# Kernel optimization log

Hardware: AMD Instinct MI355X
Metric: run time of the kernel (lower is better)

## Reference

```python
import jax, jax.numpy as jnp
import numpy as np

K = 20
NEG_SLOPE = 0.2
BN_EPS = 1e-5


def knn_idx(x, k):
    # x: (B, C, N) -> neighbor indices (B, N, k) by largest negative sq-distance
    xt = jnp.swapaxes(x, 1, 2)                      # (B, N, C)
    inner = 2.0 * jnp.einsum('bic,bjc->bij', xt, xt)
    sq = jnp.sum(xt * xt, axis=-1)                  # (B, N)
    dist = inner - sq[:, :, None] - sq[:, None, :]  # -||xi-xj||^2
    _, idx = jax.lax.top_k(dist, k)
    return idx


def edge_feature(x, src, idx):
    # x: (B, C, N) centers; src: (B, C, M) gather source; idx: (B, N, k)
    xt = jnp.swapaxes(x, 1, 2)                      # (B, N, C)
    st = jnp.swapaxes(src, 1, 2)                    # (B, M, C)
    b = jnp.arange(xt.shape[0])[:, None, None]
    neigh = st[b, idx]                              # (B, N, k, C)
    center = xt[:, :, None, :]                      # (B, N, 1, C)
    feat = jnp.concatenate(
        [neigh - center, jnp.broadcast_to(center, neigh.shape)], axis=-1)
    return jnp.transpose(feat, (0, 3, 1, 2))        # (B, 2C, N, k)


def conv_bn_lrelu(x, w, gamma, beta):
    # 1x1 conv (no bias) + training-mode BatchNorm2d + LeakyReLU(0.2)
    y = jnp.einsum('oc,bcnk->bonk', w, x)
    mean = jnp.mean(y, axis=(0, 2, 3), keepdims=True)
    var = jnp.var(y, axis=(0, 2, 3), keepdims=True)
    y = (y - mean) * jax.lax.rsqrt(var + BN_EPS)
    y = y * gamma[None, :, None, None] + beta[None, :, None, None]
    return jnp.where(y >= 0, y, NEG_SLOPE * y)


def knn_ia_idx(x, y, k):
    # cosine-similarity KNN from x (B,Cx,N) into y (B,Cy,M), normalize over channels
    xn = x / jnp.maximum(jnp.linalg.norm(x, axis=1, keepdims=True), 1e-12)
    yn = y / jnp.maximum(jnp.linalg.norm(y, axis=1, keepdims=True), 1e-12)
    simi = jnp.einsum('bci,bcj->bij', xn, yn)       # (B, N, M)
    _, idx = jax.lax.top_k(simi, k)
    return idx


def setup_inputs() -> dict:
    key = jax.random.key(0)
    ks = jax.random.split(key, 8)
    B, N, M, EMB = 8, 1024, 1024, 512
    x = jax.random.normal(ks[0], (B, 3, N), dtype=jnp.float32)
    y = jax.random.normal(ks[1], (B, 128, M), dtype=jnp.float32)
    def w(k_, o, c):
        return jax.random.normal(k_, (o, c), dtype=jnp.float32) * (1.0 / np.sqrt(c))
    inp = {
        'x': x, 'y': y,
        'w1': w(ks[2], 64, 6),
        'w2': w(ks[3], 64, 128),
        'w3': w(ks[4], 128, 128),
        'w4': w(ks[5], 256, 256),
        'w5': w(ks[6], EMB, 512),
        'g1': jnp.ones(64), 'b1': jnp.zeros(64),
        'g2': jnp.ones(64), 'b2': jnp.zeros(64),
        'g3': jnp.ones(128), 'b3': jnp.zeros(128),
        'g4': jnp.ones(256), 'b4': jnp.zeros(256),
        'g5': jnp.ones(EMB), 'b5': jnp.zeros(EMB),
    }
    return inp


def reference(x, y, w1, w2, w3, w4, w5, g1, b1, g2, b2, g3, b3, g4, b4, g5, b5):
    # block 1
    h = conv_bn_lrelu(edge_feature(x, x, knn_idx(x, K)), w1, g1, b1)
    x1 = jnp.max(h, axis=-1)                        # (B, 64, N)
    # block 2
    h = conv_bn_lrelu(edge_feature(x1, x1, knn_idx(x1, K)), w2, g2, b2)
    x2 = jnp.max(h, axis=-1)                        # (B, 64, N)
    # block 3
    h = conv_bn_lrelu(edge_feature(x2, x2, knn_idx(x2, K)), w3, g3, b3)
    x3 = jnp.max(h, axis=-1)                        # (B, 128, N)
    # block 4: cross-attention KNN into y (cosine similarity)
    h = conv_bn_lrelu(edge_feature(x3, y, knn_ia_idx(x3, y, K)), w4, g4, b4)
    x4 = jnp.max(h, axis=-1)                        # (B, 256, N)
    # final 1x1 conv + BN + LeakyReLU on concatenated features (512 ch)
    cat = jnp.concatenate([x1, x2, x3, x4], axis=1)  # (B, 512, N)
    out = conv_bn_lrelu(cat[..., None], w5, g5, b5)[..., 0]
    return out                                       # (B, n_emb_dims, N)
```

## Files before the change

kernel.cpp:

```cpp
#include <hip/hip_runtime.h>
#include <hip/hip_bf16.h>

#define KNN 20
#define NEG_SLOPE 0.2f

constexpr int BB = 8;
constexpr int NN = 1024;
constexpr int MM = 1024;

typedef short bf16x8 __attribute__((ext_vector_type(8)));
typedef float f32x4 __attribute__((ext_vector_type(4)));

__device__ __forceinline__ unsigned pack_key(double d, int j) {
  float f = (float)d;
  unsigned u = __float_as_uint(f);
  u = (u & 0x80000000u) ? ~u : (u | 0x80000000u);
  return (u & ~1023u) | (unsigned)(1023 - j);
}

__device__ __forceinline__ void topk_exact_f64(double (&v)[16], int lane, int* op) {
  for (int r = 0; r < KNN; ++r) {
    double bv = -INFINITY;
    int bj = MM;
#pragma unroll
    for (int m = 0; m < 16; ++m) {
      if (v[m] > bv) { bv = v[m]; bj = m * 64 + lane; }
    }
#pragma unroll
    for (int off = 32; off > 0; off >>= 1) {
      double ov = __shfl_xor(bv, off, 64);
      int oj = __shfl_xor(bj, off, 64);
      if (ov > bv || (ov == bv && oj < bj)) { bv = ov; bj = oj; }
    }
    if (bj < MM && lane == (bj & 63)) v[bj >> 6] = -INFINITY;
    if (lane == 0) op[r] = bj;
  }
}

__device__ __forceinline__ bool topk20_fast(unsigned (&s)[16], int lane, int* op) {
#pragma unroll
  for (int p = 1; p < 16; p <<= 1) {
#pragma unroll
    for (int k = p; k >= 1; k >>= 1) {
#pragma unroll
      for (int j = k % p; j + k < 16; j += 2 * k) {
#pragma unroll
        for (int i = 0; i < k; ++i) {
          int a = j + i, b = j + i + k;
          if (b < 16 && (a / (2 * p)) == (b / (2 * p))) {
            unsigned hi = s[a] > s[b] ? s[a] : s[b];
            unsigned lo = s[a] > s[b] ? s[b] : s[a];
            s[a] = hi;
            s[b] = lo;
          }
        }
      }
    }
  }
  unsigned prev = 0;
#pragma unroll
  for (int r = 0; r < KNN; ++r) {
    unsigned win = s[0];
#pragma unroll
    for (int off = 32; off > 0; off >>= 1) {
      unsigned o = __shfl_xor(win, off, 64);
      win = o > win ? o : win;
    }
    if (lane == 0) op[r] = 1023 - (int)(win & 1023u);
    if (s[0] == win) {
#pragma unroll
      for (int i = 0; i < 15; ++i) s[i] = s[i + 1];
      s[15] = 0u;
    }
    prev = win;
  }
  unsigned win21 = s[0];
#pragma unroll
  for (int off = 32; off > 0; off >>= 1) {
    unsigned o = __shfl_xor(win21, off, 64);
    win21 = o > win21 ? o : win21;
  }
  return (prev >> 10) == (win21 >> 10);
}

__global__ __launch_bounds__(256) void k_transpose_d(
    const float* __restrict__ in, double* __restrict__ out, int C, int Np) {
  int total = BB * C * Np;
  for (int t = blockIdx.x * 256 + threadIdx.x; t < total; t += gridDim.x * 256) {
    int c = t % C;
    int n = (t / C) % Np;
    int b = t / (C * Np);
    out[t] = (double)in[((size_t)b * C + c) * Np + n];
  }
}

__global__ __launch_bounds__(256) void k_cvt_bf16(
    const float* __restrict__ in, __hip_bfloat16* __restrict__ out, int n) {
  int i = blockIdx.x * 256 + threadIdx.x;
  if (i < n) out[i] = __float2bfloat16(in[i]);
}

template <int RECIP>
__global__ __launch_bounds__(256) void k_rowsq(
    const double* __restrict__ A, int ld, int C, double* __restrict__ sq) {
  int p = blockIdx.x * 256 + threadIdx.x;
  if (p >= BB * NN) return;
  const double* row = A + (size_t)p * ld;
  double s = 0.0;
  for (int c = 0; c < C; ++c) { double v = row[c]; s += v * v; }
  if (RECIP) {
    sq[p] = 1.0 / fmax(sqrt(s), 1e-12);
  } else {
    sq[p] = s;
  }
}

__global__ __launch_bounds__(256) void k_knn3(
    const double* __restrict__ xs3, const double* __restrict__ sq, int* __restrict__ idx) {
  __shared__ double P[NN * 3];
  int b = blockIdx.x;
  const double* Xb = xs3 + (size_t)b * NN * 3;
  int tid = threadIdx.x;
  for (int t = tid; t < NN * 3; t += 256) P[t] = Xb[t];
  __syncthreads();
  int wave = tid >> 6, lane = tid & 63;
  int i = blockIdx.y * 4 + wave;
  double xi = P[i * 3], yi = P[i * 3 + 1], zi = P[i * 3 + 2];
  double sqi = sq[b * NN + i];
  double v[16];
  unsigned s[16];
#pragma unroll
  for (int m = 0; m < 16; ++m) {
    int j = m * 64 + lane;
    double d = fma(xi, P[j * 3], 0.0);
    d = fma(yi, P[j * 3 + 1], d);
    d = fma(zi, P[j * 3 + 2], d);
    v[m] = 2.0 * d - sqi - sq[b * NN + j];
    s[m] = pack_key(v[m], j);
  }
  int* op = idx + ((size_t)b * NN + i) * KNN;
  if (topk20_fast(s, lane, op)) topk_exact_f64(v, lane, op);
}

template <int MODE>
__global__ __launch_bounds__(256) void k_gram2(
    const double* __restrict__ A, int lda, const double* __restrict__ Bm, int ldb,
    const double* __restrict__ sqA, const double* __restrict__ sqB,
    double* __restrict__ D, unsigned* __restrict__ kk, int C, int b0) {
  __shared__ double As[16][137];
  __shared__ double Bs[16][73];
  int bg = b0 + blockIdx.x;
  int bl = blockIdx.x;
  int j0 = blockIdx.y * 64;
  int i0 = blockIdx.z * 128;
  const double* Ab = A + (size_t)bg * NN * lda;
  const double* Bb = Bm + (size_t)bg * MM * ldb;
  int tx = threadIdx.x, ty = threadIdx.y;
  int tid = ty * 16 + tx;
  double acc[8][4] = {};
  for (int c0 = 0; c0 < C; c0 += 16) {
    for (int r = 0; r < 2; ++r) {
      int li = tid + r * 256;
      int row = li >> 2;
      int f = (li & 3) * 4;
      const double* ap = &Ab[(size_t)(i0 + row) * lda + c0 + f];
      double2 a0 = *(const double2*)ap;
      double2 a1 = *(const double2*)(ap + 2);
      As[f + 0][row] = a0.x;
      As[f + 1][row] = a0.y;
      As[f + 2][row] = a1.x;
      As[f + 3][row] = a1.y;
    }
    {
      int row = tid >> 2;
      int f = (tid & 3) * 4;
      const double* bp = &Bb[(size_t)(j0 + row) * ldb + c0 + f];
      double2 b0v = *(const double2*)bp;
      double2 b1v = *(const double2*)(bp + 2);
      Bs[f + 0][row] = b0v.x;
      Bs[f + 1][row] = b0v.y;
      Bs[f + 2][row] = b1v.x;
      Bs[f + 3][row] = b1v.y;
    }
    __syncthreads();
#pragma unroll
    for (int k = 0; k < 16; ++k) {
      double a_[8], b_[4];
#pragma unroll
      for (int ii = 0; ii < 8; ++ii) a_[ii] = As[k][ty * 8 + ii];
#pragma unroll
      for (int jj = 0; jj < 4; ++jj) b_[jj] = Bs[k][jj * 16 + tx];
#pragma unroll
      for (int ii = 0; ii < 8; ++ii)
#pragma unroll
        for (int jj = 0; jj < 4; ++jj)
          acc[ii][jj] = fma(a_[ii], b_[jj], acc[ii][jj]);
    }
    __syncthreads();
  }
  for (int ii = 0; ii < 8; ++ii) {
    int i = i0 + ty * 8 + ii;
    for (int jj = 0; jj < 4; ++jj) {
      int j = j0 + jj * 16 + tx;
      double r = acc[ii][jj];
      if (MODE == 1) r = 2.0 * r - sqA[bg * NN + i] - sqB[bg * NN + j];
      if (MODE == 2) r = r * sqA[bg * NN + i] * sqB[bg * NN + j];
      size_t o = ((size_t)bl * NN + i) * MM + j;
      D[o] = r;
      kk[o] = pack_key(r, j);
    }
  }
}

__global__ __launch_bounds__(256) void k_gram_sym(
    const double* __restrict__ A, int lda, const double* __restrict__ sqA,
    double* __restrict__ D, unsigned* __restrict__ kk, int C, int b0) {
  __shared__ double As[16][69];
  __shared__ double Bs[16][69];
  __shared__ double T[64][65];
  int p = blockIdx.y;
  int r = (int)((sqrtf(8.f * p + 1.f) - 1.f) * 0.5f);
  while ((r + 1) * (r + 2) / 2 <= p) ++r;
  while (r * (r + 1) / 2 > p) --r;
  int cc = p - r * (r + 1) / 2;
  int i0 = r * 64, j0 = cc * 64;
  int bg = b0 + blockIdx.x;
  int bl = blockIdx.x;
  const double* Ab = A + (size_t)bg * NN * lda;
  int tx = threadIdx.x, ty = threadIdx.y;
  int tid = ty * 16 + tx;
  double acc[4][4] = {};
  for (int c0 = 0; c0 < C; c0 += 16) {
    for (int rr = 0; rr < 4; ++rr) {
      int li = tid + rr * 256;
      int row = li >> 4, k = li & 15;
      int c = c0 + k;
      As[k][row] = (c < C) ? Ab[(size_t)(i0 + row) * lda + c] : 0.0;
      Bs[k][row] = (c < C) ? Ab[(size_t)(j0 + row) * lda + c] : 0.0;
    }
    __syncthreads();
#pragma unroll
    for (int k = 0; k < 16; ++k) {
      double a_[4], b_[4];
#pragma unroll
      for (int ii = 0; ii < 4; ++ii) a_[ii] = As[k][ty * 4 + ii];
#pragma unroll
      for (int jj = 0; jj < 4; ++jj) b_[jj] = Bs[k][jj * 16 + tx];
#pragma unroll
      for (int ii = 0; ii < 4; ++ii)
#pragma unroll
        for (int jj = 0; jj < 4; ++jj)
          acc[ii][jj] = fma(a_[ii], b_[jj], acc[ii][jj]);
    }
    __syncthreads();
  }
  for (int ii = 0; ii < 4; ++ii) {
    int i = i0 + ty * 4 + ii;
    for (int jj = 0; jj < 4; ++jj) {
      int j = j0 + jj * 16 + tx;
      double v = 2.0 * acc[ii][jj] - sqA[bg * NN + i] - sqA[bg * NN + j];
      size_t o = ((size_t)bl * NN + i) * MM + j;
      D[o] = v;
      kk[o] = pack_key(v, j);
      T[jj * 16 + tx][ty * 4 + ii] = v;
    }
  }
  if (i0 != j0) {
    __syncthreads();
    for (int rr = 0; rr < 16; ++rr) {
      int li = tid + rr * 256;
      int jrow = li >> 6, il = li & 63;
      double v = T[jrow][il];
      size_t o = ((size_t)bl * NN + j0 + jrow) * MM + i0 + il;
      D[o] = v;
      kk[o] = pack_key(v, i0 + il);
    }
  }
}

__global__ __launch_bounds__(256) void k_topk(const unsigned* __restrict__ kk,
                                              const double* __restrict__ D,
                                              int* __restrict__ idx, int b0) {
  int wave = threadIdx.x >> 6;
  int lane = threadIdx.x & 63;
  int bl = blockIdx.x;
  int row = blockIdx.y * 4 + wave;
  const unsigned* rp = kk + ((size_t)bl * NN + row) * MM;
  unsigned s[16];
#pragma unroll
  for (int m = 0; m < 16; ++m) s[m] = rp[m * 64 + lane];
  int* op = idx + ((size_t)(b0 + bl) * NN + row) * KNN;
  if (topk20_fast(s, lane, op)) {
    const double* dp = D + ((size_t)bl * NN + row) * MM;
    double v[16];
#pragma unroll
    for (int m = 0; m < 16; ++m) v[m] = dp[m * 64 + lane];
    topk_exact_f64(v, lane, op);
  }
}

__global__ __launch_bounds__(256) void k_featmm2(
    const double* __restrict__ src0, int ld0, int Np0,
    const double* __restrict__ src1, int ld1,
    const float* __restrict__ w, int CW,
    double* __restrict__ out0, double* __restrict__ out1, int C, int O) {
  __shared__ double As[16][68];
  __shared__ double Ws[16][68];
  int nbo = O >> 6;
  int b = blockIdx.x;
  int mode = blockIdx.y >= nbo;
  int o0 = (blockIdx.y - (mode ? nbo : 0)) * 64;
  int j0 = blockIdx.z * 64;
  const double* src = mode ? src1 : src0;
  int lds_ = mode ? ld1 : ld0;
  int Np = mode ? NN : Np0;
  double* out = mode ? out1 : out0;
  int tx = threadIdx.x, ty = threadIdx.y;
  int tid = ty * 16 + tx;
  const double* Sb = src + (size_t)b * Np * lds_;
  double acc[4][4] = {};
  for (int c0 = 0; c0 < C; c0 += 16) {
    for (int r = 0; r < 4; ++r) {
      int li = tid + r * 256;
      int row = li >> 4, k = li & 15;
      int c = c0 + k;
      As[k][row] = (c < C) ? Sb[(size_t)(j0 + row) * lds_ + c] : 0.0;
      double wv = 0.0;
      if (c < C) {
        const float* wr = w + (size_t)(o0 + row) * CW;
        wv = (mode == 0) ? (double)wr[c] : ((double)wr[C + c] - (double)wr[c]);
      }
      Ws[k][row] = wv;
    }
    __syncthreads();
#pragma unroll
    for (int k = 0; k < 16; ++k) {
      double a_[4], b_[4];
#pragma unroll
      for (int ii = 0; ii < 4; ++ii) a_[ii] = As[k][ty * 4 + ii];
#pragma unroll
      for (int jj = 0; jj < 4; ++jj) b_[jj] = Ws[k][tx * 4 + jj];
#pragma unroll
      for (int ii = 0; ii < 4; ++ii)
#pragma unroll
        for (int jj = 0; jj < 4; ++jj)
          acc[ii][jj] = fma(a_[ii], b_[jj], acc[ii][jj]);
    }
    __syncthreads();
  }
  for (int ii = 0; ii < 4; ++ii) {
    int j = j0 + ty * 4 + ii;
    double* op = &out[((size_t)b * Np + j) * O + o0 + tx * 4];
    double2 v0, v1;
    v0.x = acc[ii][0];
    v0.y = acc[ii][1];
    v1.x = acc[ii][2];
    v1.y = acc[ii][3];
    *(double2*)op = v0;
    *(double2*)(op + 2) = v1;
  }
}

__global__ __launch_bounds__(256) void k_gemm5_mfma(
    const __hip_bfloat16* __restrict__ cath, const __hip_bfloat16* __restrict__ w5h,
    float* __restrict__ out) {
  int b = blockIdx.x;
  int j0 = blockIdx.y * 16;
  int o0 = blockIdx.z * 64 + (threadIdx.x >> 6) * 16;
  int lane = threadIdx.x & 63;
  int m = lane & 15;
  int quad = lane >> 4;
  const __hip_bfloat16* arow = cath + ((size_t)b * NN + j0 + m) * 512 + quad * 8;
  const __hip_bfloat16* brow = w5h + (size_t)(o0 + m) * 512 + quad * 8;
  f32x4 acc = {0.f, 0.f, 0.f, 0.f};
#pragma unroll
  for (int c0 = 0; c0 < 512; c0 += 32) {
    bf16x8 a = *(const bf16x8*)(arow + c0);
    bf16x8 bb = *(const bf16x8*)(brow + c0);
    acc = __builtin_amdgcn_mfma_f32_16x16x32_bf16(a, bb, acc, 0, 0, 0);
  }
  float* obase = &out[((size_t)b * NN + j0 + quad * 4) * 512 + o0 + m];
#pragma unroll
  for (int r = 0; r < 4; ++r) obase[(size_t)r * 512] = acc[r];
}

__global__ __launch_bounds__(256) void k_gather(
    const double* __restrict__ u, const double* __restrict__ t, const int* __restrict__ idx,
    double* __restrict__ stats, double* __restrict__ mx, int O, int srcNp) {
  __shared__ int lidx[16 * KNN];
  __shared__ double rs[256];
  __shared__ double rq[256];
  int b = blockIdx.x;
  int n0 = blockIdx.y * 16;
  int o0 = blockIdx.z * 64;
  int tid = threadIdx.x;
  int lane = tid & 63, nsl = tid >> 6;
  for (int w = tid; w < 16 * KNN; w += 256)
    lidx[w] = idx[((size_t)b * NN + n0) * KNN + w];
  __syncthreads();
  int oo = o0 + lane;
  double s1 = 0.0, s2 = 0.0;
  for (int ns = nsl; ns < 16; ns += 4) {
    size_t row = (size_t)b * NN + n0 + ns;
    double tv = t[row * O + oo];
    double mxv = -INFINITY;
    double a1 = 0.0, a2 = 0.0;
#pragma unroll
    for (int k = 0; k < KNN; ++k) {
      int j = lidx[ns * KNN + k];
      double yv = u[((size_t)b * srcNp + j) * O + oo] + tv;
      mxv = fmax(mxv, yv);
      a1 += yv;
      a2 = fma(yv, yv, a2);
    }
    mx[row * O + oo] = mxv;
    s1 += a1;
    s2 += a2;
  }
  rs[tid] = s1;
  rq[tid] = s2;
  __syncthreads();
  if (tid < 64) {
    s1 = rs[tid] + rs[tid + 64] + rs[tid + 128] + rs[tid + 192];
    s2 = rq[tid] + rq[tid + 64] + rq[tid + 128] + rq[tid + 192];
    atomicAdd(&stats[o0 + tid], s1);
    atomicAdd(&stats[O + o0 + tid], s2);
  }
}

__global__ void k_bnfin(const double* __restrict__ stats, const float* __restrict__ gamma,
                        const float* __restrict__ beta, double* __restrict__ sc,
                        int O, double cnt) {
  int o = threadIdx.x;
  if (o >= O) return;
  double mean = stats[o] / cnt;
  double var = stats[O + o] / cnt - mean * mean;
  if (var < 0.0) var = 0.0;
  double rstd = 1.0 / sqrt(var + 1e-5);
  double s = (double)gamma[o] * rstd;
  double c = (double)beta[o] - mean * s;
  sc[o] = s;
  sc[O + o] = c;
}

__global__ __launch_bounds__(256) void k_bnapply(
    const double* __restrict__ mx, const double* __restrict__ u, const double* __restrict__ t,
    const int* __restrict__ idx, const double* __restrict__ sc, double* __restrict__ catd,
    __hip_bfloat16* __restrict__ cath, int coff, int O, int srcNp) {
  int i = blockIdx.x * 256 + threadIdx.x;
  int total = BB * NN * O;
  if (i >= total) return;
  int oo = i % O;
  int n = (i / O) % NN;
  int b = i / (O * NN);
  double s = sc[oo], c = sc[O + oo];
  double v;
  if (s >= 0.0) {
    v = mx[i];
  } else {
    double tv = t[i];
    double mn = INFINITY;
    for (int k = 0; k < KNN; ++k) {
      int j = idx[((size_t)b * NN + n) * KNN + k];
      mn = fmin(mn, u[((size_t)b * srcNp + j) * O + oo] + tv);
    }
    v = mn;
  }
  double a = s * v + c;
  a = (a >= 0.0) ? a : 0.2 * a;
  size_t ci = ((size_t)b * NN + n) * 512 + coff + oo;
  cath[ci] = __float2bfloat16((float)a);
  if (coff < 256) catd[((size_t)b * NN + n) * 256 + coff + oo] = a;
}

__global__ __launch_bounds__(256) void k_stats512(
    const float* __restrict__ y5, double* __restrict__ stats) {
  int b = blockIdx.y;
  int n0 = blockIdx.x * 32;
  int tid = threadIdx.x;
  for (int part = 0; part < 2; ++part) {
    int oo = tid + part * 256;
    float a1 = 0.f, a2 = 0.f;
    for (int ns = 0; ns < 32; ++ns) {
      float v = y5[((size_t)b * NN + n0 + ns) * 512 + oo];
      a1 += v;
      a2 = fmaf(v, v, a2);
    }
    atomicAdd(&stats[oo], (double)a1);
    atomicAdd(&stats[512 + oo], (double)a2);
  }
}

__global__ __launch_bounds__(256) void k_final5b(
    const float* __restrict__ y5, const double* __restrict__ sc, float* __restrict__ out) {
  __shared__ float tile[64][65];
  int b = blockIdx.z;
  int n0 = blockIdx.x * 64;
  int o0 = blockIdx.y * 64;
  int tid = threadIdx.x;
  for (int r = 0; r < 16; ++r) {
    int li = tid + r * 256;
    int nl = li >> 6, ol = li & 63;
    float v = y5[((size_t)b * NN + n0 + nl) * 512 + o0 + ol];
    float a = (float)(sc[o0 + ol] * (double)v + sc[512 + o0 + ol]);
    a = (a >= 0.f) ? a : NEG_SLOPE * a;
    tile[nl][ol] = a;
  }
  __syncthreads();
  for (int r = 0; r < 16; ++r) {
    int li = tid + r * 256;
    int ol = li >> 6, nl = li & 63;
    out[((size_t)b * 512 + o0 + ol) * NN + n0 + nl] = tile[nl][ol];
  }
}

extern "C" void kernel_launch(void* const* d_in, const int* in_sizes, int n_in,
                              void* d_out, int out_size, void* d_ws, size_t ws_size,
                              hipStream_t stream) {
  const float* x = (const float*)d_in[0];
  const float* y = (const float*)d_in[1];
  const float* w1 = (const float*)d_in[2];
  const float* w2 = (const float*)d_in[3];
  const float* w3 = (const float*)d_in[4];
  const float* w4 = (const float*)d_in[5];
  const float* w5 = (const float*)d_in[6];
  const float* g1 = (const float*)d_in[7];
  const float* b1 = (const float*)d_in[8];
  const float* g2 = (const float*)d_in[9];
  const float* b2 = (const float*)d_in[10];
  const float* g3 = (const float*)d_in[11];
  const float* b3 = (const float*)d_in[12];
  const float* g4 = (const float*)d_in[13];
  const float* b4 = (const float*)d_in[14];
  const float* g5 = (const float*)d_in[15];
  const float* b5 = (const float*)d_in[16];

  char* base = (char*)d_ws;
  size_t off = 0;
  auto alloc = [&](size_t bytes) -> char* {
    char* p = base + off;
    off += (bytes + 255) & ~(size_t)255;
    return p;
  };
  double* st = (double*)alloc(1024 * 8);
  double* sc = (double*)alloc(1024 * 8);
  double* sq = (double*)alloc((size_t)BB * NN * 8);
  double* rnx = (double*)alloc((size_t)BB * NN * 8);
  double* rny = (double*)alloc((size_t)BB * MM * 8);
  int* idxb = (int*)alloc((size_t)BB * NN * KNN * 4);
  double* xs3d = (double*)alloc((size_t)BB * NN * 3 * 8);
  double* ysd = (double*)alloc((size_t)BB * MM * 128 * 8);
  double* catd = (double*)alloc((size_t)BB * NN * 256 * 8);
  __hip_bfloat16* cath = (__hip_bfloat16*)alloc((size_t)BB * NN * 512 * 2);
  __hip_bfloat16* w5h = (__hip_bfloat16*)alloc((size_t)512 * 512 * 2);
  double* uu = (double*)alloc((size_t)BB * MM * 256 * 8);
  double* tt = (double*)alloc((size_t)BB * NN * 256 * 8);
  size_t ddBatchBytes = (size_t)NN * MM * 8;
  size_t kkBatchBytes = (size_t)NN * MM * 4;
  size_t avail = (ws_size > off) ? (ws_size - off) : 0;
  int CB = (int)(avail / (ddBatchBytes + kkBatchBytes));
  if (CB < 1) CB = 1;
  if (CB > BB) CB = BB;
  char* U = alloc((size_t)CB * ddBatchBytes);
  unsigned* KK = (unsigned*)alloc((size_t)CB * kkBatchBytes);
  double* DD = (double*)U;
  float* y5 = (float*)uu;
  double* mx = (double*)d_out;
  float* outp = (float*)d_out;

  const dim3 blk2(16, 16);
  const double cntE = (double)BB * NN * KNN;

  auto knn = [&](const double* A, int lda, const double* Bm, int ldb,
                 const double* sa, const double* sb, int C, int mode, int sym) {
    for (int b0 = 0; b0 < BB; b0 += CB) {
      int cb = (BB - b0 < CB) ? (BB - b0) : CB;
      if (sym) {
        k_gram_sym<<<dim3(cb, 136), blk2, 0, stream>>>(A, lda, sa, DD, KK, C, b0);
      } else {
        dim3 g(cb, MM / 64, NN / 128);
        if (mode == 1)
          k_gram2<1><<<g, blk2, 0, stream>>>(A, lda, Bm, ldb, sa, sb, DD, KK, C, b0);
        else
          k_gram2<2><<<g, blk2, 0, stream>>>(A, lda, Bm, ldb, sa, sb, DD, KK, C, b0);
      }
      k_topk<<<dim3(cb, 256), 256, 0, stream>>>(KK, DD, idxb, b0);
    }
  };

  auto edge_layer = [&](const double* ctr, int ldc, const double* src, int ldsrc,
                        int srcNp, const float* w, int CW, const float* g,
                        const float* bb, int C, int O, int coff) {
    k_featmm2<<<dim3(8, 2 * (O / 64), 16), blk2, 0, stream>>>(src, ldsrc, srcNp, ctr,
                                                              ldc, w, CW, uu, tt, C, O);
    hipMemsetAsync(st, 0, 1024 * 8, stream);
    k_gather<<<dim3(BB, NN / 16, O / 64), 256, 0, stream>>>(uu, tt, idxb, st, mx, O,
                                                            srcNp);
    k_bnfin<<<1, O, 0, stream>>>(st, g, bb, sc, O, cntE);
    k_bnapply<<<(BB * NN * O + 255) / 256, 256, 0, stream>>>(mx, uu, tt, idxb, sc, catd,
                                                             cath, coff, O, srcNp);
  };

  k_transpose_d<<<96, 256, 0, stream>>>(x, xs3d, 3, NN);
  k_transpose_d<<<2048, 256, 0, stream>>>(y, ysd, 128, MM);
  k_cvt_bf16<<<1024, 256, 0, stream>>>(w5, w5h, 512 * 512);

  k_rowsq<0><<<32, 256, 0, stream>>>(xs3d, 3, 3, sq);
  k_knn3<<<dim3(BB, 256), 256, 0, stream>>>(xs3d, sq, idxb);
  edge_layer(xs3d, 3, xs3d, 3, NN, w1, 6, g1, b1, 3, 64, 0);

  k_rowsq<0><<<32, 256, 0, stream>>>(catd, 256, 64, sq);
  knn(catd, 256, catd, 256, sq, sq, 64, 1, 1);
  edge_layer(catd, 256, catd, 256, NN, w2, 128, g2, b2, 64, 64, 64);

  k_rowsq<0><<<32, 256, 0, stream>>>(catd + 64, 256, 64, sq);
  knn(catd + 64, 256, catd + 64, 256, sq, sq, 64, 1, 1);
  edge_layer(catd + 64, 256, catd + 64, 256, NN, w3, 128, g3, b3, 64, 128, 128);

  k_rowsq<1><<<32, 256, 0, stream>>>(catd + 128, 256, 128, rnx);
  k_rowsq<1><<<32, 256, 0, stream>>>(ysd, 128, 128, rny);
  knn(catd + 128, 256, ysd, 128, rnx, rny, 128, 2, 0);
  edge_layer(catd + 128, 256, ysd, 128, MM, w4, 256, g4, b4, 128, 256, 256);

  hipMemsetAsync(st, 0, 1024 * 8, stream);
  k_gemm5_mfma<<<dim3(BB, 64, 8), 256, 0, stream>>>(cath, w5h, y5);
  k_stats512<<<dim3(32, 8), 256, 0, stream>>>(y5, st);
  k_bnfin<<<1, 512, 0, stream>>>(st, g5, b5, sc, 512, (double)(BB * NN));
  k_final5b<<<dim3(16, 8, 8), 256, 0, stream>>>(y5, sc, outp);
}
```

Measured before the change: 719.5 us.

## Use FP64 MFMA for KNN gram and recompute exact distances in top-k fallback

Replaces the FP64 FMA gram kernels (including the symmetric variant) with one kernel that uses the 16x16x4 FP64 MFMA instruction. The output lane layout is found at runtime by a probe kernel, and the old FMA path is kept as a fallback. The full double-precision distance matrix is no longer written. The exact top-k fallback instead recomputes the needed row of distances from the input features, which cuts global memory traffic and frees workspace for larger batch chunks. The cost is giving up the symmetric-tile saving, adding two tiny probe launches, and doing redundant row recomputation whenever the fast path fails.

```diff
diff --git a/kernel.cpp b/kernel.cpp
--- a/kernel.cpp
+++ b/kernel.cpp
@@ -10,6 +10,7 @@
 
 typedef short bf16x8 __attribute__((ext_vector_type(8)));
 typedef float f32x4 __attribute__((ext_vector_type(4)));
+typedef double f64x4 __attribute__((ext_vector_type(4)));
 
 __device__ __forceinline__ unsigned pack_key(double d, int j) {
   float f = (float)d;
@@ -81,6 +82,45 @@
     win21 = o > win21 ? o : win21;
   }
   return (prev >> 10) == (win21 >> 10);
+}
+
+__global__ void k_probe_mfma(double* __restrict__ p) {
+  int lane = threadIdx.x & 63;
+  f64x4 z = {0.0, 0.0, 0.0, 0.0};
+  double ai = (double)(lane & 15);
+  double p3 = 1.0, p5 = 1.0;
+  int kq = lane >> 4;
+  for (int t = 0; t < kq; ++t) { p3 *= 3.0; p5 *= 5.0; }
+  f64x4 d1 = __builtin_amdgcn_mfma_f64_16x16x4f64(ai, 1.0, z, 0, 0, 0);
+  f64x4 d2 = __builtin_amdgcn_mfma_f64_16x16x4f64(1.0, ai, z, 0, 0, 0);
+  f64x4 d3 = __builtin_amdgcn_mfma_f64_16x16x4f64(p3, p5, z, 0, 0, 0);
+#pragma unroll
+  for (int r = 0; r < 4; ++r) {
+    p[lane * 4 + r] = d1[r];
+    p[256 + lane * 4 + r] = d2[r];
+    p[512 + lane * 4 + r] = d3[r];
+  }
+}
+
+__global__ void k_probe_decode(const double* __restrict__ p, int* __restrict__ rowt,
+                               int* __restrict__ colt, int* __restrict__ flag) {
+  if (threadIdx.x != 0 || blockIdx.x != 0) return;
+  unsigned char seen[256];
+  for (int e = 0; e < 256; ++e) seen[e] = 0;
+  bool ok = true;
+  for (int e = 0; e < 256 && ok; ++e) {
+    double va = p[e], vb = p[256 + e], vp = p[512 + e];
+    int i = (int)(va * 0.25);
+    int j = (int)(vb * 0.25);
+    ok = (i >= 0) && (i < 16) && (j >= 0) && (j < 16) && (va == 4.0 * (double)i) &&
+         (vb == 4.0 * (double)j) && (vp == 3616.0) && (seen[i * 16 + j] == 0);
+    if (ok) {
+      seen[i * 16 + j] = 1;
+      rowt[e] = i;
+      colt[e] = j;
+    }
+  }
+  *flag = ok ? 1 : 0;
 }
 
 __global__ __launch_bounds__(256) void k_transpose_d(
@@ -143,158 +183,135 @@
 }
 
 template <int MODE>
-__global__ __launch_bounds__(256) void k_gram2(
+__global__ __launch_bounds__(256) void k_gram_u(
     const double* __restrict__ A, int lda, const double* __restrict__ Bm, int ldb,
     const double* __restrict__ sqA, const double* __restrict__ sqB,
-    double* __restrict__ D, unsigned* __restrict__ kk, int C, int b0) {
-  __shared__ double As[16][137];
-  __shared__ double Bs[16][73];
+    unsigned* __restrict__ kk, int C, int b0, const int* __restrict__ rowt,
+    const int* __restrict__ colt, const int* __restrict__ flag) {
+  __shared__ double As[16][66];
+  __shared__ double Bs[16][66];
   int bg = b0 + blockIdx.x;
   int bl = blockIdx.x;
   int j0 = blockIdx.y * 64;
-  int i0 = blockIdx.z * 128;
+  int i0 = blockIdx.z * 64;
   const double* Ab = A + (size_t)bg * NN * lda;
   const double* Bb = Bm + (size_t)bg * MM * ldb;
-  int tx = threadIdx.x, ty = threadIdx.y;
-  int tid = ty * 16 + tx;
-  double acc[8][4] = {};
-  for (int c0 = 0; c0 < C; c0 += 16) {
-    for (int r = 0; r < 2; ++r) {
-      int li = tid + r * 256;
-      int row = li >> 2;
-      int f = (li & 3) * 4;
-      const double* ap = &Ab[(size_t)(i0 + row) * lda + c0 + f];
-      double2 a0 = *(const double2*)ap;
-      double2 a1 = *(const double2*)(ap + 2);
-      As[f + 0][row] = a0.x;
-      As[f + 1][row] = a0.y;
-      As[f + 2][row] = a1.x;
-      As[f + 3][row] = a1.y;
-    }
-    {
-      int row = tid >> 2;
-      int f = (tid & 3) * 4;
-      const double* bp = &Bb[(size_t)(j0 + row) * ldb + c0 + f];
-      double2 b0v = *(const double2*)bp;
-      double2 b1v = *(const double2*)(bp + 2);
-      Bs[f + 0][row] = b0v.x;
-      Bs[f + 1][row] = b0v.y;
-      Bs[f + 2][row] = b1v.x;
-      Bs[f + 3][row] = b1v.y;
-    }
-    __syncthreads();
-#pragma unroll
-    for (int k = 0; k < 16; ++k) {
-      double a_[8], b_[4];
-#pragma unroll
-      for (int ii = 0; ii < 8; ++ii) a_[ii] = As[k][ty * 8 + ii];
-#pragma unroll
-      for (int jj = 0; jj < 4; ++jj) b_[jj] = Bs[k][jj * 16 + tx];
-#pragma unroll
-      for (int ii = 0; ii < 8; ++ii)
-#pragma unroll
-        for (int jj = 0; jj < 4; ++jj)
-          acc[ii][jj] = fma(a_[ii], b_[jj], acc[ii][jj]);
-    }
-    __syncthreads();
-  }
-  for (int ii = 0; ii < 8; ++ii) {
-    int i = i0 + ty * 8 + ii;
-    for (int jj = 0; jj < 4; ++jj) {
-      int j = j0 + jj * 16 + tx;
-      double r = acc[ii][jj];
-      if (MODE == 1) r = 2.0 * r - sqA[bg * NN + i] - sqB[bg * NN + j];
-      if (MODE == 2) r = r * sqA[bg * NN + i] * sqB[bg * NN + j];
-      size_t o = ((size_t)bl * NN + i) * MM + j;
-      D[o] = r;
-      kk[o] = pack_key(r, j);
-    }
-  }
-}
-
-__global__ __launch_bounds__(256) void k_gram_sym(
-    const double* __restrict__ A, int lda, const double* __restrict__ sqA,
-    double* __restrict__ D, unsigned* __restrict__ kk, int C, int b0) {
-  __shared__ double As[16][69];
-  __shared__ double Bs[16][69];
-  __shared__ double T[64][65];
-  int p = blockIdx.y;
-  int r = (int)((sqrtf(8.f * p + 1.f) - 1.f) * 0.5f);
-  while ((r + 1) * (r + 2) / 2 <= p) ++r;
-  while (r * (r + 1) / 2 > p) --r;
-  int cc = p - r * (r + 1) / 2;
-  int i0 = r * 64, j0 = cc * 64;
-  int bg = b0 + blockIdx.x;
-  int bl = blockIdx.x;
-  const double* Ab = A + (size_t)bg * NN * lda;
-  int tx = threadIdx.x, ty = threadIdx.y;
-  int tid = ty * 16 + tx;
-  double acc[4][4] = {};
-  for (int c0 = 0; c0 < C; c0 += 16) {
-    for (int rr = 0; rr < 4; ++rr) {
-      int li = tid + rr * 256;
-      int row = li >> 4, k = li & 15;
-      int c = c0 + k;
-      As[k][row] = (c < C) ? Ab[(size_t)(i0 + row) * lda + c] : 0.0;
-      Bs[k][row] = (c < C) ? Ab[(size_t)(j0 + row) * lda + c] : 0.0;
-    }
-    __syncthreads();
-#pragma unroll
-    for (int k = 0; k < 16; ++k) {
-      double a_[4], b_[4];
-#pragma unroll
-      for (int ii = 0; ii < 4; ++ii) a_[ii] = As[k][ty * 4 + ii];
-#pragma unroll
-      for (int jj = 0; jj < 4; ++jj) b_[jj] = Bs[k][jj * 16 + tx];
-#pragma unroll
-      for (int ii = 0; ii < 4; ++ii)
-#pragma unroll
-        for (int jj = 0; jj < 4; ++jj)
-          acc[ii][jj] = fma(a_[ii], b_[jj], acc[ii][jj]);
-    }
-    __syncthreads();
-  }
-  for (int ii = 0; ii < 4; ++ii) {
-    int i = i0 + ty * 4 + ii;
-    for (int jj = 0; jj < 4; ++jj) {
-      int j = j0 + jj * 16 + tx;
-      double v = 2.0 * acc[ii][jj] - sqA[bg * NN + i] - sqA[bg * NN + j];
-      size_t o = ((size_t)bl * NN + i) * MM + j;
-      D[o] = v;
-      kk[o] = pack_key(v, j);
-      T[jj * 16 + tx][ty * 4 + ii] = v;
-    }
-  }
-  if (i0 != j0) {
-    __syncthreads();
-    for (int rr = 0; rr < 16; ++rr) {
-      int li = tid + rr * 256;
-      int jrow = li >> 6, il = li & 63;
-      double v = T[jrow][il];
-      size_t o = ((size_t)bl * NN + j0 + jrow) * MM + i0 + il;
-      D[o] = v;
-      kk[o] = pack_key(v, i0 + il);
-    }
-  }
-}
-
-__global__ __launch_bounds__(256) void k_topk(const unsigned* __restrict__ kk,
-                                              const double* __restrict__ D,
-                                              int* __restrict__ idx, int b0) {
+  int tid = threadIdx.x;
+  if (*flag) {
+    int lane = tid & 63, w = tid >> 6;
+    int lm = lane & 15, lq = lane >> 4;
+    f64x4 acc[4] = {};
+    for (int c0 = 0; c0 < C; c0 += 16) {
+      if (c0) __syncthreads();
+      for (int r = 0; r < 4; ++r) {
+        int li = tid + r * 256;
+        int row = li >> 4, k = li & 15;
+        As[k][row] = Ab[(size_t)(i0 + row) * lda + c0 + k];
+        Bs[k][row] = Bb[(size_t)(j0 + row) * ldb + c0 + k];
+      }
+      __syncthreads();
+#pragma unroll
+      for (int kc = 0; kc < 4; ++kc) {
+        double a = As[kc * 4 + lq][w * 16 + lm];
+#pragma unroll
+        for (int t = 0; t < 4; ++t) {
+          double b = Bs[kc * 4 + lq][t * 16 + lm];
+          acc[t] = __builtin_amdgcn_mfma_f64_16x16x4f64(a, b, acc[t], 0, 0, 0);
+        }
+      }
+    }
+    int rta[4], cta[4];
+#pragma unroll
+    for (int r = 0; r < 4; ++r) {
+      rta[r] = rowt[lane * 4 + r];
+      cta[r] = colt[lane * 4 + r];
+    }
+#pragma unroll
+    for (int t = 0; t < 4; ++t) {
+#pragma unroll
+      for (int r = 0; r < 4; ++r) {
+        int i = i0 + w * 16 + rta[r];
+        int j = j0 + t * 16 + cta[r];
+        double v = acc[t][r];
+        if (MODE == 1) v = 2.0 * v - sqA[(size_t)bg * NN + i] - sqB[(size_t)bg * MM + j];
+        if (MODE == 2) v = v * sqA[(size_t)bg * NN + i] * sqB[(size_t)bg * MM + j];
+        kk[((size_t)bl * NN + i) * MM + j] = pack_key(v, j);
+      }
+    }
+  } else {
+    int tx = tid & 15, ty = tid >> 4;
+    double acc[4][4] = {};
+    for (int c0 = 0; c0 < C; c0 += 16) {
+      if (c0) __syncthreads();
+      for (int r = 0; r < 4; ++r) {
+        int li = tid + r * 256;
+        int row = li >> 4, k = li & 15;
+        As[k][row] = Ab[(size_t)(i0 + row) * lda + c0 + k];
+        Bs[k][row] = Bb[(size_t)(j0 + row) * ldb + c0 + k];
+      }
+      __syncthreads();
+#pragma unroll
+      for (int k = 0; k < 16; ++k) {
+        double a_[4], b_[4];
+#pragma unroll
+        for (int ii = 0; ii < 4; ++ii) a_[ii] = As[k][ty * 4 + ii];
+#pragma unroll
+        for (int jj = 0; jj < 4; ++jj) b_[jj] = Bs[k][jj * 16 + tx];
+#pragma unroll
+        for (int ii = 0; ii < 4; ++ii)
+#pragma unroll
+          for (int jj = 0; jj < 4; ++jj)
+            acc[ii][jj] = fma(a_[ii], b_[jj], acc[ii][jj]);
+      }
+    }
+    for (int ii = 0; ii < 4; ++ii) {
+      int i = i0 + ty * 4 + ii;
+      double qa = sqA[(size_t)bg * NN + i];
+      for (int jj = 0; jj < 4; ++jj) {
+        int j = j0 + jj * 16 + tx;
+        double v = acc[ii][jj];
+        if (MODE == 1) v = 2.0 * v - qa - sqB[(size_t)bg * MM + j];
+        if (MODE == 2) v = v * qa * sqB[(size_t)bg * MM + j];
+        kk[((size_t)bl * NN + i) * MM + j] = pack_key(v, j);
+      }
+    }
+  }
+}
+
+template <int MODE>
+__global__ __launch_bounds__(256) void k_topk(
+    const unsigned* __restrict__ kk, const double* __restrict__ A, int lda,
+    const double* __restrict__ Bm, int ldb, const double* __restrict__ sqA,
+    const double* __restrict__ sqB, int C, int* __restrict__ idx, int b0) {
   int wave = threadIdx.x >> 6;
   int lane = threadIdx.x & 63;
   int bl = blockIdx.x;
+  int bg = b0 + bl;
   int row = blockIdx.y * 4 + wave;
   const unsigned* rp = kk + ((size_t)bl * NN + row) * MM;
   unsigned s[16];
 #pragma unroll
   for (int m = 0; m < 16; ++m) s[m] = rp[m * 64 + lane];
-  int* op = idx + ((size_t)(b0 + bl) * NN + row) * KNN;
+  int* op = idx + ((size_t)bg * NN + row) * KNN;
   if (topk20_fast(s, lane, op)) {
-    const double* dp = D + ((size_t)bl * NN + row) * MM;
+    const double* ar = A + ((size_t)bg * NN + row) * lda;
+    const double* Bb = Bm + (size_t)bg * MM * ldb;
+    double qa = sqA[(size_t)bg * NN + row];
     double v[16];
 #pragma unroll
-    for (int m = 0; m < 16; ++m) v[m] = dp[m * 64 + lane];
+    for (int m = 0; m < 16; ++m) v[m] = 0.0;
+    for (int c = 0; c < C; ++c) {
+      double av = ar[c];
+#pragma unroll
+      for (int m = 0; m < 16; ++m)
+        v[m] = fma(av, Bb[(size_t)(m * 64 + lane) * ldb + c], v[m]);
+    }
+#pragma unroll
+    for (int m = 0; m < 16; ++m) {
+      double qb = sqB[(size_t)bg * MM + m * 64 + lane];
+      if (MODE == 1) v[m] = 2.0 * v[m] - qa - qb;
+      if (MODE == 2) v[m] = v[m] * qa * qb;
+    }
     topk_exact_f64(v, lane, op);
   }
 }
@@ -548,6 +565,10 @@
   double* rnx = (double*)alloc((size_t)BB * NN * 8);
   double* rny = (double*)alloc((size_t)BB * MM * 8);
   int* idxb = (int*)alloc((size_t)BB * NN * KNN * 4);
+  double* pout = (double*)alloc(3 * 256 * 8);
+  int* rowt = (int*)alloc(256 * 4);
+  int* colt = (int*)alloc(256 * 4);
+  int* pflag = (int*)alloc(256);
   double* xs3d = (double*)alloc((size_t)BB * NN * 3 * 8);
   double* ysd = (double*)alloc((size_t)BB * MM * 128 * 8);
   double* catd = (double*)alloc((size_t)BB * NN * 256 * 8);
@@ -555,15 +576,12 @@
   __hip_bfloat16* w5h = (__hip_bfloat16*)alloc((size_t)512 * 512 * 2);
   double* uu = (double*)alloc((size_t)BB * MM * 256 * 8);
   double* tt = (double*)alloc((size_t)BB * NN * 256 * 8);
-  size_t ddBatchBytes = (size_t)NN * MM * 8;
   size_t kkBatchBytes = (size_t)NN * MM * 4;
   size_t avail = (ws_size > off) ? (ws_size - off) : 0;
-  int CB = (int)(avail / (ddBatchBytes + kkBatchBytes));
+  int CB = (int)(avail / kkBatchBytes);
   if (CB < 1) CB = 1;
   if (CB > BB) CB = BB;
-  char* U = alloc((size_t)CB * ddBatchBytes);
   unsigned* KK = (unsigned*)alloc((size_t)CB * kkBatchBytes);
-  double* DD = (double*)U;
   float* y5 = (float*)uu;
   double* mx = (double*)d_out;
   float* outp = (float*)d_out;
@@ -572,19 +590,21 @@
   const double cntE = (double)BB * NN * KNN;
 
   auto knn = [&](const double* A, int lda, const double* Bm, int ldb,
-                 const double* sa, const double* sb, int C, int mode, int sym) {
+                 const double* sa, const double* sb, int C, int mode) {
     for (int b0 = 0; b0 < BB; b0 += CB) {
       int cb = (BB - b0 < CB) ? (BB - b0) : CB;
-      if (sym) {
-        k_gram_sym<<<dim3(cb, 136), blk2, 0, stream>>>(A, lda, sa, DD, KK, C, b0);
+      dim3 g(cb, MM / 64, NN / 64);
+      if (mode == 1) {
+        k_gram_u<1><<<g, 256, 0, stream>>>(A, lda, Bm, ldb, sa, sb, KK, C, b0, rowt,
+                                           colt, pflag);
+        k_topk<1><<<dim3(cb, 256), 256, 0, stream>>>(KK, A, lda, Bm, ldb, sa, sb, C,
+                                                     idxb, b0);
       } else {
-        dim3 g(cb, MM / 64, NN / 128);
-        if (mode == 1)
-          k_gram2<1><<<g, blk2, 0, stream>>>(A, lda, Bm, ldb, sa, sb, DD, KK, C, b0);
-        else
-          k_gram2<2><<<g, blk2, 0, stream>>>(A, lda, Bm, ldb, sa, sb, DD, KK, C, b0);
-      }
-      k_topk<<<dim3(cb, 256), 256, 0, stream>>>(KK, DD, idxb, b0);
+        k_gram_u<2><<<g, 256, 0, stream>>>(A, lda, Bm, ldb, sa, sb, KK, C, b0, rowt,
+                                           colt, pflag);
+        k_topk<2><<<dim3(cb, 256), 256, 0, stream>>>(KK, A, lda, Bm, ldb, sa, sb, C,
+                                                     idxb, b0);
+      }
     }
   };
 
@@ -601,6 +621,8 @@
                                                              cath, coff, O, srcNp);
   };
 
+  k_probe_mfma<<<1, 64, 0, stream>>>(pout);
+  k_probe_decode<<<1, 1, 0, stream>>>(pout, rowt, colt, pflag);
   k_transpose_d<<<96, 256, 0, stream>>>(x, xs3d, 3, NN);
   k_transpose_d<<<2048, 256, 0, stream>>>(y, ysd, 128, MM);
   k_cvt_bf16<<<1024, 256, 0, stream>>>(w5, w5h, 512 * 512);
@@ -610,16 +632,16 @@
   edge_layer(xs3d, 3, xs3d, 3, NN, w1, 6, g1, b1, 3, 64, 0);
 
   k_rowsq<0><<<32, 256, 0, stream>>>(catd, 256, 64, sq);
-  knn(catd, 256, catd, 256, sq, sq, 64, 1, 1);
+  knn(catd, 256, catd, 256, sq, sq, 64, 1);
   edge_layer(catd, 256, catd, 256, NN, w2, 128, g2, b2, 64, 64, 64);
 
   k_rowsq<0><<<32, 256, 0, stream>>>(catd + 64, 256, 64, sq);
-  knn(catd + 64, 256, catd + 64, 256, sq, sq, 64, 1, 1);
+  knn(catd + 64, 256, catd + 64, 256, sq, sq, 64, 1);
   edge_layer(catd + 64, 256, catd + 64, 256, NN, w3, 128, g3, b3, 64, 128, 128);
 
   k_rowsq<1><<<32, 256, 0, stream>>>(catd + 128, 256, 128, rnx);
   k_rowsq<1><<<32, 256, 0, stream>>>(ysd, 128, 128, rny);
-  knn(catd + 128, 256, ysd, 128, rnx, rny, 128, 2, 0);
+  knn(catd + 128, 256, ysd, 128, rnx, rny, 128, 2);
   edge_layer(catd + 128, 256, ysd, 128, MM, w4, 256, g4, b4, 128, 256, 256);
 
   hipMemsetAsync(st, 0, 1024 * 8, stream);
```

After: 1.015 ms. 1.41x slower.
